# Performance work log

Measured on AMD Instinct MI355X. Metric: run time of the kernel, lower is better.

Reference implementation:

```python
import jax, jax.numpy as jnp
import numpy as np

N, E, IN_DIM, HID, OUT = 50000, 800000, 128, 128, 64


def setup_inputs() -> dict:
    key = jax.random.key(0)
    k = jax.random.split(key, 6)
    h = jax.random.normal(k[0], (N, IN_DIM), dtype=jnp.float32)
    edge_index = jax.random.randint(k[1], (2, E), 0, N, dtype=jnp.int64)
    s_in, s_hid = 1.0 / np.sqrt(IN_DIM), 1.0 / np.sqrt(HID)
    W_gcn = jax.random.uniform(k[2], (IN_DIM, HID), jnp.float32, -s_in, s_in)
    b_gcn = jnp.zeros((HID,), jnp.float32)
    W_fc = jax.random.uniform(k[3], (HID, OUT), jnp.float32, -s_hid, s_hid)
    b_fc = jax.random.uniform(k[4], (OUT,), jnp.float32, -s_hid, s_hid)
    return {"h": h, "edge_index": edge_index, "W_gcn": W_gcn,
            "b_gcn": b_gcn, "W_fc": W_fc, "b_fc": b_fc}


def reference(h, edge_index, W_gcn, b_gcn, W_fc, b_fc):
    n = h.shape[0]
    # GCNConv: transform, add self-loops, symmetric normalization, scatter-add
    x = h @ W_gcn                                   # [N, HID]
    loop = jnp.arange(n, dtype=edge_index.dtype)
    row = jnp.concatenate([edge_index[0], loop])    # source nodes
    col = jnp.concatenate([edge_index[1], loop])    # destination nodes
    deg = jax.ops.segment_sum(jnp.ones_like(col, dtype=x.dtype), col,
                              num_segments=n)       # in-degree incl. self-loop
    dinv = jnp.where(deg > 0, jax.lax.rsqrt(deg), 0.0)
    norm = dinv[row] * dinv[col]                    # [E+N]
    msg = x[row] * norm[:, None]                    # gather + scale
    agg = jax.ops.segment_sum(msg, col, num_segments=n) + b_gcn
    # ReLU then projection
    return jax.nn.relu(agg) @ W_fc + b_fc
```

## Files before the change

### kernel.cpp

```cpp
#include <hip/hip_runtime.h>

#define N_NODES 50000
#define N_EDGES 800000
#define NBKT 196
#define BCAP 6144
#define UTS 136

typedef __attribute__((ext_vector_type(4))) float floatx4;
typedef __attribute__((ext_vector_type(8))) _Float16 half8;
typedef __attribute__((ext_vector_type(2))) _Float16 half2v;

#define O_PTR   0UL
#define O_GF    200192UL
#define O_DINV  201472UL
#define O_ESRC  401664UL
#define O_W1    3801856UL
#define O_W2    3834624UL
#define O_STG   3851008UL
#define O_H16   16651008UL

__global__ __launch_bounds__(256) void k_binA(const int* __restrict__ ei,
                                              int* __restrict__ gfill,
                                              unsigned* __restrict__ staging) {
    __shared__ int cnt[NBKT];
    __shared__ int gbase[NBKT];
    __shared__ int s_i64;
    int t = threadIdx.x;
    if (t < 64) {
        unsigned w = ((const unsigned*)ei)[2 * t + 1];
        unsigned long long m = __ballot(w == 0u);
        if (t == 0) s_i64 = (__popcll(m) >= 60) ? 1 : 0;
    }
    for (int i = t; i < NBKT; i += 256) cnt[i] = 0;
    __syncthreads();
    bool i64 = s_i64 != 0;
    int e0 = blockIdx.x * 4096 + t * 16;
    int sv[16], dvv[16];
    if (i64) {
        const int4* ps = (const int4*)(ei) + (e0 >> 1);
        const int4* pd = (const int4*)(ei + 2 * (size_t)N_EDGES) + (e0 >> 1);
#pragma unroll
        for (int g = 0; g < 8; ++g) {
            if (e0 + 2 * g < N_EDGES) {
                int4 s4 = ps[g], d4 = pd[g];
                sv[2 * g] = s4.x; sv[2 * g + 1] = s4.z;
                dvv[2 * g] = d4.x; dvv[2 * g + 1] = d4.z;
            } else { dvv[2 * g] = -1; dvv[2 * g + 1] = -1; }
        }
    } else {
        const int4* ps = (const int4*)(ei) + (e0 >> 2);
        const int4* pd = (const int4*)(ei + (size_t)N_EDGES) + (e0 >> 2);
#pragma unroll
        for (int g = 0; g < 4; ++g) {
            if (e0 + 4 * g < N_EDGES) {
                int4 s4 = ps[g], d4 = pd[g];
                sv[4 * g] = s4.x; sv[4 * g + 1] = s4.y; sv[4 * g + 2] = s4.z; sv[4 * g + 3] = s4.w;
                dvv[4 * g] = d4.x; dvv[4 * g + 1] = d4.y; dvv[4 * g + 2] = d4.z; dvv[4 * g + 3] = d4.w;
            } else { dvv[4 * g] = -1; dvv[4 * g + 1] = -1; dvv[4 * g + 2] = -1; dvv[4 * g + 3] = -1; }
        }
    }
    unsigned pk[16]; int rk[16]; short bk[16];
#pragma unroll
    for (int j = 0; j < 16; ++j) {
        int d = dvv[j];
        if (d >= 0 && e0 + j < N_EDGES) {
            int b = d >> 8;
            bk[j] = (short)b;
            pk[j] = (unsigned)sv[j] | ((unsigned)(d & 255) << 16);
            rk[j] = atomicAdd(&cnt[b], 1);
        } else bk[j] = -1;
    }
    __syncthreads();
    for (int i = t; i < NBKT; i += 256)
        gbase[i] = atomicAdd(&gfill[i], cnt[i]);
    __syncthreads();
#pragma unroll
    for (int j = 0; j < 16; ++j) {
        if (bk[j] >= 0) {
            int pos = gbase[bk[j]] + rk[j];
            if (pos < BCAP) staging[(size_t)bk[j] * BCAP + pos] = pk[j];
        }
    }
}

__global__ __launch_bounds__(256) void k_binB(const unsigned* __restrict__ staging,
                                              const int* __restrict__ gfill,
                                              const float* __restrict__ h,
                                              const float* __restrict__ Wg,
                                              const float* __restrict__ Wf,
                                              int* __restrict__ ptr,
                                              float* __restrict__ dinv,
                                              _Float16* __restrict__ h16,
                                              _Float16* __restrict__ W1,
                                              _Float16* __restrict__ W2,
                                              int* __restrict__ esrc) {
    __shared__ unsigned se[BCAP];
    __shared__ int lcnt[256];
    __shared__ int lscan[256];
    __shared__ int cur[256];
    __shared__ float sdinv[256];
    __shared__ int s_cb;
    int b = blockIdx.x, t = threadIdx.x;
    if (b < 64) {
        int i = b * 256 + t;
        int n = i >> 7, k = i & 127;
        W1[i] = (_Float16)Wg[k * 128 + n];
    } else if (b < 96) {
        int i = (b - 64) * 256 + t;
        int n = i >> 7, k = i & 127;
        W2[i] = (_Float16)Wf[k * 64 + n];
    }
    int nbase = b * 256;
    int nn = min(256, N_NODES - nbase);
    int cnt = min(gfill[b], BCAP);
    if (t < 64) {
        int acc = 0;
        for (int i = t; i < b; i += 64) acc += min(gfill[i], BCAP);
#pragma unroll
        for (int off = 32; off > 0; off >>= 1) acc += __shfl_down(acc, off);
        if (t == 0) s_cb = acc;
    }
    lcnt[t] = 0;
    __syncthreads();
    int cb = s_cb;
    const unsigned* st = staging + (size_t)b * BCAP;
    for (int i = t; i < cnt; i += 256) {
        unsigned p = st[i];
        se[i] = p;
        atomicAdd(&lcnt[p >> 16], 1);
    }
    __syncthreads();
    int v = lcnt[t];
    lscan[t] = v;
    __syncthreads();
    for (int off = 1; off < 256; off <<= 1) {
        int x = (t >= off) ? lscan[t - off] : 0;
        __syncthreads(); lscan[t] += x; __syncthreads();
    }
    int segstart = cb + (lscan[t] - v);
    float dv = rsqrtf((float)(v + 1));
    if (t < nn) {
        int node = nbase + t;
        ptr[node] = segstart;
        dinv[node] = dv;
        sdinv[t] = dv;
        cur[t] = segstart;
    }
    __syncthreads();
    for (int i = t; i < cnt; i += 256) {
        unsigned p = se[i];
        int pos = atomicAdd(&cur[p >> 16], 1);
        esrc[pos] = (int)(p & 0xffffu);
    }
    int half = t >> 7;
    int col = t & 127;
    for (int r = half; r < nn; r += 2) {
        int node = nbase + r;
        h16[(size_t)node * 128 + col] = (_Float16)(h[(size_t)node * 128 + col] * sdinv[r]);
    }
}

__global__ __launch_bounds__(256, 8) void k_aggF(const _Float16* __restrict__ h16,
                                                 const int* __restrict__ ptr,
                                                 const int* __restrict__ esrc,
                                                 const float* __restrict__ dinv,
                                                 const _Float16* __restrict__ W1,
                                                 const _Float16* __restrict__ W2,
                                                 const float* __restrict__ bg,
                                                 const float* __restrict__ bfc,
                                                 float* __restrict__ out) {
    __shared__ _Float16 ut[16 * UTS];
    __shared__ _Float16 z[16 * UTS];
    int wave = threadIdx.x >> 6;
    int lane = threadIdx.x & 63;
    int nb = blockIdx.x * 16;
    for (int q = 0; q < 4; ++q) {
        int node = nb + wave * 4 + q;
        int p0 = ptr[node];
        int p1 = (node + 1 < N_NODES) ? ptr[node + 1] : N_EDGES;
        half2v us = *(const half2v*)(h16 + (size_t)node * 128 + lane * 2);
        float a0 = (float)us[0], a1 = (float)us[1];
        for (int base = p0; base < p1; base += 64) {
            int cnt = p1 - base; if (cnt > 64) cnt = 64;
            int idx = 0;
            if (lane < cnt) idx = esrc[base + lane];
            int j = 0;
            for (; j + 8 <= cnt; j += 8) {
                int s0 = __shfl(idx, j),     s1 = __shfl(idx, j + 1);
                int s2 = __shfl(idx, j + 2), s3 = __shfl(idx, j + 3);
                int s4 = __shfl(idx, j + 4), s5 = __shfl(idx, j + 5);
                int s6 = __shfl(idx, j + 6), s7 = __shfl(idx, j + 7);
                half2v u0 = *(const half2v*)(h16 + (size_t)s0 * 128 + lane * 2);
                half2v u1 = *(const half2v*)(h16 + (size_t)s1 * 128 + lane * 2);
                half2v u2 = *(const half2v*)(h16 + (size_t)s2 * 128 + lane * 2);
                half2v u3 = *(const half2v*)(h16 + (size_t)s3 * 128 + lane * 2);
                half2v u4 = *(const half2v*)(h16 + (size_t)s4 * 128 + lane * 2);
                half2v u5 = *(const half2v*)(h16 + (size_t)s5 * 128 + lane * 2);
                half2v u6 = *(const half2v*)(h16 + (size_t)s6 * 128 + lane * 2);
                half2v u7 = *(const half2v*)(h16 + (size_t)s7 * 128 + lane * 2);
                a0 += (float)u0[0] + (float)u1[0] + (float)u2[0] + (float)u3[0]
                    + (float)u4[0] + (float)u5[0] + (float)u6[0] + (float)u7[0];
                a1 += (float)u0[1] + (float)u1[1] + (float)u2[1] + (float)u3[1]
                    + (float)u4[1] + (float)u5[1] + (float)u6[1] + (float)u7[1];
            }
            for (; j + 4 <= cnt; j += 4) {
                int s0 = __shfl(idx, j),     s1 = __shfl(idx, j + 1);
                int s2 = __shfl(idx, j + 2), s3 = __shfl(idx, j + 3);
                half2v u0 = *(const half2v*)(h16 + (size_t)s0 * 128 + lane * 2);
                half2v u1 = *(const half2v*)(h16 + (size_t)s1 * 128 + lane * 2);
                half2v u2 = *(const half2v*)(h16 + (size_t)s2 * 128 + lane * 2);
                half2v u3 = *(const half2v*)(h16 + (size_t)s3 * 128 + lane * 2);
                a0 += (float)u0[0] + (float)u1[0] + (float)u2[0] + (float)u3[0];
                a1 += (float)u0[1] + (float)u1[1] + (float)u2[1] + (float)u3[1];
            }
            for (; j < cnt; ++j) {
                int s = __shfl(idx, j);
                half2v uu = *(const half2v*)(h16 + (size_t)s * 128 + lane * 2);
                a0 += (float)uu[0]; a1 += (float)uu[1];
            }
        }
        float sc = dinv[node];
        int r = wave * 4 + q;
        ut[r * UTS + lane * 2]     = (_Float16)(a0 * sc);
        ut[r * UTS + lane * 2 + 1] = (_Float16)(a1 * sc);
    }
    __syncthreads();
    int quad = lane >> 4, l15 = lane & 15;
    half8 a[4];
#pragma unroll
    for (int kk = 0; kk < 4; ++kk)
        a[kk] = *(const half8*)(ut + l15 * UTS + kk * 32 + quad * 8);
#pragma unroll
    for (int tt = 0; tt < 2; ++tt) {
        floatx4 acc = {0.f, 0.f, 0.f, 0.f};
        int n = (wave * 2 + tt) * 16 + l15;
#pragma unroll
        for (int kk = 0; kk < 4; ++kk) {
            half8 bb = *(const half8*)(W1 + n * 128 + kk * 32 + quad * 8);
            acc = __builtin_amdgcn_mfma_f32_16x16x32_f16(a[kk], bb, acc, 0, 0, 0);
        }
        float bias = bg[n];
#pragma unroll
        for (int i = 0; i < 4; ++i)
            z[(quad * 4 + i) * UTS + n] = (_Float16)fmaxf(acc[i] + bias, 0.f);
    }
    __syncthreads();
    half8 a2[4];
#pragma unroll
    for (int kk = 0; kk < 4; ++kk)
        a2[kk] = *(const half8*)(z + l15 * UTS + kk * 32 + quad * 8);
    {
        floatx4 acc = {0.f, 0.f, 0.f, 0.f};
        int n = wave * 16 + l15;
#pragma unroll
        for (int kk = 0; kk < 4; ++kk) {
            half8 bb = *(const half8*)(W2 + n * 128 + kk * 32 + quad * 8);
            acc = __builtin_amdgcn_mfma_f32_16x16x32_f16(a2[kk], bb, acc, 0, 0, 0);
        }
        float bias = bfc[n];
#pragma unroll
        for (int i = 0; i < 4; ++i)
            out[(size_t)(nb + quad * 4 + i) * 64 + n] = acc[i] + bias;
    }
}

extern "C" void kernel_launch(void* const* d_in, const int* in_sizes, int n_in,
                              void* d_out, int out_size, void* d_ws, size_t ws_size,
                              hipStream_t stream) {
    (void)in_sizes; (void)n_in; (void)out_size; (void)ws_size;
    const float* h  = (const float*)d_in[0];
    const int*   ei = (const int*)d_in[1];
    const float* Wg = (const float*)d_in[2];
    const float* bg = (const float*)d_in[3];
    const float* Wf = (const float*)d_in[4];
    const float* bf = (const float*)d_in[5];
    float* out = (float*)d_out;

    char* ws = (char*)d_ws;
    int*      ptr   = (int*)(ws + O_PTR);
    int*      gfill = (int*)(ws + O_GF);
    float*    dinv  = (float*)(ws + O_DINV);
    int*      esrc  = (int*)(ws + O_ESRC);
    _Float16* W1    = (_Float16*)(ws + O_W1);
    _Float16* W2    = (_Float16*)(ws + O_W2);
    unsigned* staging = (unsigned*)(ws + O_STG);
    _Float16* h16   = (_Float16*)(ws + O_H16);

    hipMemsetAsync(gfill, 0, NBKT * sizeof(int), stream);
    k_binA<<<NBKT, 256, 0, stream>>>(ei, gfill, staging);
    k_binB<<<NBKT, 256, 0, stream>>>(staging, gfill, h, Wg, Wf,
                                     ptr, dinv, h16, W1, W2, esrc);
    k_aggF<<<N_NODES / 16, 256, 0, stream>>>(h16, ptr, esrc, dinv,
                                             W1, W2, bg, bf, out);
}
```

Baseline: 157.3 us.

## Rebalance binning kernels: global degree atomics, separate h16 conversion blocks

The edge-binning kernel now runs twice as many blocks, each handling half as many edges, plus extra blocks that transpose and convert the weights. It also counts in-degree with global atomics into a new deg array. The second kernel splits its work: bucket blocks only build CSR pointers and edge sources, while a separate set of blocks computes dinv from deg and converts h to fp16 with vectorized float4 loads. The goal is more parallelism, and to take the large h conversion off the critical path of the bucket scan, at the cost of 800k extra global atomics and a larger memset.

```diff
diff --git a/kernel.cpp b/kernel.cpp
--- a/kernel.cpp
+++ b/kernel.cpp
@@ -5,27 +5,48 @@
 #define NBKT 196
 #define BCAP 6144
 #define UTS 136
+#define GBIN 392
 
 typedef __attribute__((ext_vector_type(4))) float floatx4;
 typedef __attribute__((ext_vector_type(8))) _Float16 half8;
+typedef __attribute__((ext_vector_type(4))) _Float16 half4;
 typedef __attribute__((ext_vector_type(2))) _Float16 half2v;
 
 #define O_PTR   0UL
 #define O_GF    200192UL
-#define O_DINV  201472UL
-#define O_ESRC  401664UL
+#define O_DEG   201472UL
+#define O_DINV  401664UL
+#define O_ESRC  601856UL
 #define O_W1    3801856UL
 #define O_W2    3834624UL
 #define O_STG   3851008UL
-#define O_H16   16651008UL
+#define O_H16   8667904UL
 
 __global__ __launch_bounds__(256) void k_binA(const int* __restrict__ ei,
                                               int* __restrict__ gfill,
-                                              unsigned* __restrict__ staging) {
+                                              unsigned* __restrict__ staging,
+                                              int* __restrict__ deg,
+                                              const float* __restrict__ Wg,
+                                              const float* __restrict__ Wf,
+                                              _Float16* __restrict__ W1,
+                                              _Float16* __restrict__ W2) {
+    int b = blockIdx.x, t = threadIdx.x;
+    if (b >= GBIN) {
+        int wb = b - GBIN;
+        if (wb < 64) {
+            int i = wb * 256 + t;
+            int n = i >> 7, k = i & 127;
+            W1[i] = (_Float16)Wg[k * 128 + n];
+        } else {
+            int i = (wb - 64) * 256 + t;
+            int n = i >> 7, k = i & 127;
+            W2[i] = (_Float16)Wf[k * 64 + n];
+        }
+        return;
+    }
     __shared__ int cnt[NBKT];
     __shared__ int gbase[NBKT];
     __shared__ int s_i64;
-    int t = threadIdx.x;
     if (t < 64) {
         unsigned w = ((const unsigned*)ei)[2 * t + 1];
         unsigned long long m = __ballot(w == 0u);
@@ -34,13 +55,13 @@
     for (int i = t; i < NBKT; i += 256) cnt[i] = 0;
     __syncthreads();
     bool i64 = s_i64 != 0;
-    int e0 = blockIdx.x * 4096 + t * 16;
-    int sv[16], dvv[16];
+    int e0 = b * 2048 + t * 8;
+    int sv[8], dvv[8];
     if (i64) {
         const int4* ps = (const int4*)(ei) + (e0 >> 1);
         const int4* pd = (const int4*)(ei + 2 * (size_t)N_EDGES) + (e0 >> 1);
 #pragma unroll
-        for (int g = 0; g < 8; ++g) {
+        for (int g = 0; g < 4; ++g) {
             if (e0 + 2 * g < N_EDGES) {
                 int4 s4 = ps[g], d4 = pd[g];
                 sv[2 * g] = s4.x; sv[2 * g + 1] = s4.z;
@@ -51,7 +72,7 @@
         const int4* ps = (const int4*)(ei) + (e0 >> 2);
         const int4* pd = (const int4*)(ei + (size_t)N_EDGES) + (e0 >> 2);
 #pragma unroll
-        for (int g = 0; g < 4; ++g) {
+        for (int g = 0; g < 2; ++g) {
             if (e0 + 4 * g < N_EDGES) {
                 int4 s4 = ps[g], d4 = pd[g];
                 sv[4 * g] = s4.x; sv[4 * g + 1] = s4.y; sv[4 * g + 2] = s4.z; sv[4 * g + 3] = s4.w;
@@ -59,15 +80,16 @@
             } else { dvv[4 * g] = -1; dvv[4 * g + 1] = -1; dvv[4 * g + 2] = -1; dvv[4 * g + 3] = -1; }
         }
     }
-    unsigned pk[16]; int rk[16]; short bk[16];
-#pragma unroll
-    for (int j = 0; j < 16; ++j) {
+    unsigned pk[8]; int rk[8]; short bk[8];
+#pragma unroll
+    for (int j = 0; j < 8; ++j) {
         int d = dvv[j];
         if (d >= 0 && e0 + j < N_EDGES) {
-            int b = d >> 8;
-            bk[j] = (short)b;
+            int bkt = d >> 8;
+            bk[j] = (short)bkt;
             pk[j] = (unsigned)sv[j] | ((unsigned)(d & 255) << 16);
-            rk[j] = atomicAdd(&cnt[b], 1);
+            rk[j] = atomicAdd(&cnt[bkt], 1);
+            atomicAdd(&deg[d], 1);
         } else bk[j] = -1;
     }
     __syncthreads();
@@ -75,7 +97,7 @@
         gbase[i] = atomicAdd(&gfill[i], cnt[i]);
     __syncthreads();
 #pragma unroll
-    for (int j = 0; j < 16; ++j) {
+    for (int j = 0; j < 8; ++j) {
         if (bk[j] >= 0) {
             int pos = gbase[bk[j]] + rk[j];
             if (pos < BCAP) staging[(size_t)bk[j] * BCAP + pos] = pk[j];
@@ -85,31 +107,41 @@
 
 __global__ __launch_bounds__(256) void k_binB(const unsigned* __restrict__ staging,
                                               const int* __restrict__ gfill,
+                                              const int* __restrict__ deg,
                                               const float* __restrict__ h,
-                                              const float* __restrict__ Wg,
-                                              const float* __restrict__ Wf,
                                               int* __restrict__ ptr,
                                               float* __restrict__ dinv,
                                               _Float16* __restrict__ h16,
-                                              _Float16* __restrict__ W1,
-                                              _Float16* __restrict__ W2,
                                               int* __restrict__ esrc) {
+    int b = blockIdx.x, t = threadIdx.x;
+    if (b >= NBKT) {
+        __shared__ float sdv[256];
+        int nb = (b - NBKT) * 256;
+        int nn = min(256, N_NODES - nb);
+        if (t < nn) {
+            float dv = rsqrtf((float)(deg[nb + t] + 1));
+            dinv[nb + t] = dv;
+            sdv[t] = dv;
+        }
+        __syncthreads();
+        const floatx4* src = (const floatx4*)(h + (size_t)nb * 128);
+        half4* dst = (half4*)(h16 + (size_t)nb * 128);
+        int nq = nn * 32;
+        for (int i = t; i < nq; i += 256) {
+            floatx4 v = src[i];
+            float s = sdv[i >> 5];
+            half4 o;
+            o[0] = (_Float16)(v[0] * s); o[1] = (_Float16)(v[1] * s);
+            o[2] = (_Float16)(v[2] * s); o[3] = (_Float16)(v[3] * s);
+            dst[i] = o;
+        }
+        return;
+    }
     __shared__ unsigned se[BCAP];
     __shared__ int lcnt[256];
     __shared__ int lscan[256];
     __shared__ int cur[256];
-    __shared__ float sdinv[256];
     __shared__ int s_cb;
-    int b = blockIdx.x, t = threadIdx.x;
-    if (b < 64) {
-        int i = b * 256 + t;
-        int n = i >> 7, k = i & 127;
-        W1[i] = (_Float16)Wg[k * 128 + n];
-    } else if (b < 96) {
-        int i = (b - 64) * 256 + t;
-        int n = i >> 7, k = i & 127;
-        W2[i] = (_Float16)Wf[k * 64 + n];
-    }
     int nbase = b * 256;
     int nn = min(256, N_NODES - nbase);
     int cnt = min(gfill[b], BCAP);
@@ -138,12 +170,8 @@
         __syncthreads(); lscan[t] += x; __syncthreads();
     }
     int segstart = cb + (lscan[t] - v);
-    float dv = rsqrtf((float)(v + 1));
     if (t < nn) {
-        int node = nbase + t;
-        ptr[node] = segstart;
-        dinv[node] = dv;
-        sdinv[t] = dv;
+        ptr[nbase + t] = segstart;
         cur[t] = segstart;
     }
     __syncthreads();
@@ -151,12 +179,6 @@
         unsigned p = se[i];
         int pos = atomicAdd(&cur[p >> 16], 1);
         esrc[pos] = (int)(p & 0xffffu);
-    }
-    int half = t >> 7;
-    int col = t & 127;
-    for (int r = half; r < nn; r += 2) {
-        int node = nbase + r;
-        h16[(size_t)node * 128 + col] = (_Float16)(h[(size_t)node * 128 + col] * sdinv[r]);
     }
 }
 
@@ -279,6 +301,7 @@
     char* ws = (char*)d_ws;
     int*      ptr   = (int*)(ws + O_PTR);
     int*      gfill = (int*)(ws + O_GF);
+    int*      deg   = (int*)(ws + O_DEG);
     float*    dinv  = (float*)(ws + O_DINV);
     int*      esrc  = (int*)(ws + O_ESRC);
     _Float16* W1    = (_Float16*)(ws + O_W1);
@@ -286,10 +309,9 @@
     unsigned* staging = (unsigned*)(ws + O_STG);
     _Float16* h16   = (_Float16*)(ws + O_H16);
 
-    hipMemsetAsync(gfill, 0, NBKT * sizeof(int), stream);
-    k_binA<<<NBKT, 256, 0, stream>>>(ei, gfill, staging);
-    k_binB<<<NBKT, 256, 0, stream>>>(staging, gfill, h, Wg, Wf,
-                                     ptr, dinv, h16, W1, W2, esrc);
+    hipMemsetAsync(ws + O_GF, 0, (size_t)(O_DINV - O_GF), stream);
+    k_binA<<<GBIN + 96, 256, 0, stream>>>(ei, gfill, staging, deg, Wg, Wf, W1, W2);
+    k_binB<<<NBKT + 196, 256, 0, stream>>>(staging, gfill, deg, h, ptr, dinv, h16, esrc);
     k_aggF<<<N_NODES / 16, 256, 0, stream>>>(h16, ptr, esrc, dinv,
                                              W1, W2, bg, bf, out);
 }
```

Result: slower. 181.6 us (+15.4%).
